# Performance work log

Measured on AMD Instinct MI355X. Metric: run time of the kernel, lower is better.

## Reference

```python
import jax, jax.numpy as jnp
import numpy as np

N, D, H, C, L, G, E = 50000, 128, 128, 40, 3, 4, 800000
GRID = jnp.linspace(-2.0, 2.0, G)          # RBF grid on [-2, 2]
DENOM = 4.0 / (G - 1)                      # (grid_max - grid_min) / (num_grids - 1)


def _layernorm(x, g, b, eps=1e-5):
    m = x.mean(-1, keepdims=True)
    v = x.var(-1, keepdims=True)
    return (x - m) * jax.lax.rsqrt(v + eps) * g + b


def _fkan(x, ln_g, ln_b, sw, bw, bb):
    # FastKANLayer: layernorm -> Gaussian RBF basis -> bias-free spline linear, + silu base update
    xn = _layernorm(x, ln_g, ln_b)
    basis = jnp.exp(-(((xn[..., None] - GRID) / DENOM) ** 2))     # [n, d, G]
    ret = basis.reshape(x.shape[0], -1) @ sw.T                    # [n, out]
    return ret + jax.nn.silu(x) @ bw.T + bb


def _gcn_prop(h, src, dst, n):
    # symmetric GCN normalization with self-loops already appended to src/dst
    deg = jax.ops.segment_sum(jnp.ones(src.shape[0], h.dtype), dst, num_segments=n)
    dis = jnp.where(deg > 0, jax.lax.rsqrt(deg), 0.0)
    norm = dis[src] * dis[dst]                                    # [e]
    return jax.ops.segment_sum(h[src] * norm[:, None], dst, num_segments=n)


def _batchnorm(x, g, b, eps=1e-5):
    m = x.mean(0)
    v = x.var(0)  # biased variance, as torch BN uses for normalization
    return (x - m) * jax.lax.rsqrt(v + eps) * g + b


def setup_inputs() -> dict:
    key = jax.random.key(0)
    ks = jax.random.split(key, 8)
    x = jax.random.normal(ks[0], (N, D), jnp.float32)
    edge_index = jax.random.randint(ks[1], (2, E), 0, N, jnp.int64)
    return {
        "x": x,
        "edge_index": edge_index,
        "ln_g": jnp.ones((L, D), jnp.float32),
        "ln_b": jnp.zeros((L, D), jnp.float32),
        "sw": jax.random.normal(ks[2], (L, H, D * G), jnp.float32) * 0.1,
        "bw": jax.random.normal(ks[3], (L, H, D), jnp.float32) * (1.0 / np.sqrt(D)),
        "bb": jnp.zeros((L, H), jnp.float32),
        "gcn_bias": jnp.zeros((L, H), jnp.float32),
        "bn_g": jnp.ones((L, H), jnp.float32),
        "bn_b": jnp.zeros((L, H), jnp.float32),
        "ln_g_out": jnp.ones((D + L * H,), jnp.float32),
        "ln_b_out": jnp.zeros((D + L * H,), jnp.float32),
        "sw_out": jax.random.normal(ks[4], (C, (D + L * H) * G), jnp.float32) * 0.1,
        "bw_out": jax.random.normal(ks[5], (C, D + L * H), jnp.float32) * (1.0 / np.sqrt(D + L * H)),
        "bb_out": jnp.zeros((C,), jnp.float32),
    }


def reference(x, edge_index, ln_g, ln_b, sw, bw, bb, gcn_bias, bn_g, bn_b,
              ln_g_out, ln_b_out, sw_out, bw_out, bb_out):
    loops = jnp.arange(N, dtype=edge_index.dtype)
    src = jnp.concatenate([edge_index[0], loops])
    dst = jnp.concatenate([edge_index[1], loops])
    feats = [x]
    h = x
    for i in range(L):  # fixed small layer count
        h = _fkan(h, ln_g[i], ln_b[i], sw[i], bw[i], bb[i])
        h = _gcn_prop(h, src, dst, N) + gcn_bias[i]
        h = _batchnorm(h, bn_g[i], bn_b[i])
        feats.append(h)
    xcat = jnp.concatenate(feats, axis=1)  # [N, D + L*H] skip-concat
    return _fkan(xcat, ln_g_out, ln_b_out, sw_out, bw_out, bb_out)
```

## Files before the change

### kernel.cpp

```cpp
#include <hip/hip_runtime.h>
#include <hip/hip_bf16.h>

#define TPB 256

typedef __attribute__((ext_vector_type(8))) short s8v;
typedef __attribute__((ext_vector_type(4))) float f32x4;
typedef unsigned short u16;

__device__ __forceinline__ u16 f2bf(float f){
  union { __hip_bfloat16 h; u16 u; } cv;
  cv.h = __float2bfloat16(f);
  return cv.u;
}

__device__ __forceinline__ unsigned pack_bf2(float lo, float hi){
  return (unsigned)f2bf(lo) | ((unsigned)f2bf(hi) << 16);
}

__device__ __forceinline__ float bflo(unsigned u){ return __uint_as_float(u << 16); }
__device__ __forceinline__ float bfhi(unsigned u){ return __uint_as_float(u & 0xffff0000u); }

__device__ __forceinline__ float wave_sum(float v){
  #pragma unroll
  for (int off=32; off>0; off>>=1) v += __shfl_xor(v, off, 64);
  return v;
}

__device__ __forceinline__ int wave_incl_scan(int v, int lane){
  #pragma unroll
  for (int off=1; off<64; off<<=1){
    int u = __shfl_up(v, off, 64);
    if (lane >= off) v += u;
  }
  return v;
}

__global__ __launch_bounds__(TPB) void count_k(const int* __restrict__ dstE, int* __restrict__ cnt, int E){
  int e = blockIdx.x*TPB + threadIdx.x;
  if (e < E) atomicAdd(&cnt[dstE[e]], 1);
}

__global__ __launch_bounds__(TPB) void dis_k(const int* __restrict__ cnt, float* __restrict__ disp, int nN){
  int n = blockIdx.x*TPB + threadIdx.x;
  if (n < nN) disp[n] = rsqrtf((float)cnt[n] + 1.0f);
}

__global__ __launch_bounds__(TPB) void scan1_k(const int* __restrict__ cnt, int* __restrict__ rowptr,
                                               int* __restrict__ bsum, int nN){
  int t = threadIdx.x;
  int i = blockIdx.x*TPB + t;
  int lane = t & 63, wid = t >> 6;
  int v = (i < nN) ? cnt[i] : 0;
  int inc = wave_incl_scan(v, lane);
  __shared__ int wsum[4];
  if (lane == 63) wsum[wid] = inc;
  __syncthreads();
  int off = 0;
  #pragma unroll
  for (int w=0; w<4; ++w) if (w < wid) off += wsum[w];
  if (i < nN) rowptr[i] = inc - v + off;
  if (t == 0) bsum[blockIdx.x] = wsum[0]+wsum[1]+wsum[2]+wsum[3];
}

__global__ __launch_bounds__(TPB) void scan2_k(int* __restrict__ bsum, int nbk){
  int t = threadIdx.x;
  int lane = t & 63, wid = t >> 6;
  int v = (t < nbk) ? bsum[t] : 0;
  int inc = wave_incl_scan(v, lane);
  __shared__ int wsum[4];
  if (lane == 63) wsum[wid] = inc;
  __syncthreads();
  int off = 0;
  #pragma unroll
  for (int w=0; w<4; ++w) if (w < wid) off += wsum[w];
  __syncthreads();
  if (t < nbk) bsum[t] = inc - v + off;
}

__global__ __launch_bounds__(TPB) void scan3_k(int* __restrict__ rowptr, const int* __restrict__ bsum, int nN, int E){
  int i = blockIdx.x*TPB + threadIdx.x;
  if (i < nN) rowptr[i] += bsum[blockIdx.x];
  if (i == 0) rowptr[nN] = E;
}

__global__ __launch_bounds__(TPB) void fill_k(const int* __restrict__ srcE, const int* __restrict__ dstE,
                                              const int* __restrict__ rowptr, int* __restrict__ cursor,
                                              int* __restrict__ csr, int E){
  int e = blockIdx.x*TPB + threadIdx.x;
  if (e >= E) return;
  int d = dstE[e];
  int pos = atomicAdd(&cursor[d], 1);
  csr[rowptr[d] + pos] = srcE[e];
}

__global__ __launch_bounds__(TPB) void ln512_k(const float* __restrict__ x, const u16* __restrict__ hl16,
                                               const float* __restrict__ scshAll,
                                               float* __restrict__ meanp, float* __restrict__ rstdp, int nN){
  int g = blockIdx.x*TPB + threadIdx.x;
  int n = g >> 6, lane = g & 63;
  if (n >= nN) return;
  float s = 0.f, sq = 0.f;
  #pragma unroll
  for (int k=0;k<8;k++){
    float v;
    if (k < 2){
      v = x[(size_t)n*128 + lane + k*64];
    } else {
      int k2 = k - 2, li = k2 >> 1, cc = lane + (k2&1)*64;
      float raw = bflo((unsigned)hl16[((size_t)li*nN + n)*128 + cc] << 0) ;
      raw = __uint_as_float(((unsigned)hl16[((size_t)li*nN + n)*128 + cc]) << 16);
      v = fmaf(raw, scshAll[li*256 + cc], scshAll[li*256 + 128 + cc]);
    }
    s += v; sq += v*v;
  }
  s = wave_sum(s); sq = wave_sum(sq);
  float m = s * (1.f/512.f);
  float var = fmaxf(sq * (1.f/512.f) - m*m, 0.f);
  if (lane == 0){ meanp[n] = m; rstdp[n] = rsqrtf(var + 1e-5f); }
}

__global__ __launch_bounds__(TPB) void prep_wpre_k(const float* __restrict__ sw, const float* __restrict__ bw,
                                                   u16* __restrict__ wpre, int IN, int KSTEPS, int NTILES, int OUTW){
  int idx = blockIdx.x*TPB + threadIdx.x;
  if (idx >= NTILES*KSTEPS*512) return;
  int b = idx & 7, lane = (idx >> 3) & 63, rest = idx >> 9;
  int kstep = rest % KSTEPS, nt = rest / KSTEPS;
  int chunk = kstep / 5, g = kstep % 5;
  int d = chunk*32 + ((lane >> 4)*8 + b);
  int n = nt*16 + (lane & 15);
  float v = 0.f;
  if (n < OUTW) v = (g < 4) ? sw[(size_t)n*IN*4 + d*4 + g] : bw[(size_t)n*IN + d];
  wpre[idx] = f2bf(v);
}

__device__ __forceinline__ void build_frags(const float* __restrict__ h8, float mean, float rstd,
                                            const float* __restrict__ lngv, const float* __restrict__ lnbv,
                                            s8v* __restrict__ a){
  float bas[5][8];
  #pragma unroll
  for (int u=0; u<8; ++u){
    float v = h8[u];
    float xn = (v - mean)*rstd*lngv[u] + lnbv[u];
    float y = 0.75f*xn;
    float z0 = y+1.5f, z1 = y+0.5f, z2 = y-0.5f, z3 = y-1.5f;
    bas[0][u] = __expf(-z0*z0);
    bas[1][u] = __expf(-z1*z1);
    bas[2][u] = __expf(-z2*z2);
    bas[3][u] = __expf(-z3*z3);
    bas[4][u] = v * __builtin_amdgcn_rcpf(1.f + __expf(-v));
  }
  #pragma unroll
  for (int g=0; g<5; ++g){
    #pragma unroll
    for (int j=0; j<4; ++j)
      ((unsigned*)&a[g])[j] = pack_bf2(bas[g][2*j], bas[g][2*j+1]);
  }
}

template<bool BF16IN>
__global__ __launch_bounds__(TPB) void fkan_layer_k(
    const float* __restrict__ in32, const u16* __restrict__ in16,
    const float* __restrict__ scsh,
    const float* __restrict__ lng, const float* __restrict__ lnb,
    const u16* __restrict__ wpre, const float* __restrict__ bias,
    const float* __restrict__ disp, u16* __restrict__ hs, int nN)
{
  const int t = threadIdx.x;
  const int wv = blockIdx.x*(TPB/64) + (t >> 6);
  const int ngrp = (nN + 15) >> 4;
  const int ng = wv >> 1, jh = wv & 1;
  if (ng >= ngrp) return;
  const int l = t & 63, clo = l & 15, kq = l >> 4;
  const int node = ng*16 + clo;
  const int nc = node < nN ? node : nN-1;

  float h[4][8];
  #pragma unroll
  for (int c=0; c<4; ++c){
    if (BF16IN){
      uint4 raw = *(const uint4*)(in16 + (size_t)nc*128 + c*32 + kq*8);
      h[c][0]=bflo(raw.x); h[c][1]=bfhi(raw.x);
      h[c][2]=bflo(raw.y); h[c][3]=bfhi(raw.y);
      h[c][4]=bflo(raw.z); h[c][5]=bfhi(raw.z);
      h[c][6]=bflo(raw.w); h[c][7]=bfhi(raw.w);
      #pragma unroll
      for (int u=0; u<8; ++u){
        int d = c*32 + kq*8 + u;
        h[c][u] = fmaf(h[c][u], scsh[d], scsh[128 + d]);
      }
    } else {
      const float* hrow = in32 + (size_t)nc*128;
      *(float4*)&h[c][0] = *(const float4*)(hrow + c*32 + kq*8);
      *(float4*)&h[c][4] = *(const float4*)(hrow + c*32 + kq*8 + 4);
    }
  }
  float s = 0.f, sq = 0.f;
  #pragma unroll
  for (int c=0; c<4; ++c)
    #pragma unroll
    for (int u=0; u<8; ++u){ float v = h[c][u]; s += v; sq += v*v; }
  s  += __shfl_xor(s, 16, 64);  s  += __shfl_xor(s, 32, 64);
  sq += __shfl_xor(sq, 16, 64); sq += __shfl_xor(sq, 32, 64);
  float mean = s * (1.f/128.f);
  float var  = fmaxf(sq * (1.f/128.f) - mean*mean, 0.f);
  float rstd = rsqrtf(var + 1e-5f);

  f32x4 acc[4];
  #pragma unroll
  for (int j=0; j<4; ++j) acc[j] = (f32x4)0.f;

  for (int c=0; c<4; ++c){
    float lngv[8], lnbv[8];
    *(float4*)&lngv[0] = *(const float4*)(lng + c*32 + kq*8);
    *(float4*)&lngv[4] = *(const float4*)(lng + c*32 + kq*8 + 4);
    *(float4*)&lnbv[0] = *(const float4*)(lnb + c*32 + kq*8);
    *(float4*)&lnbv[4] = *(const float4*)(lnb + c*32 + kq*8 + 4);
    s8v a[5];
    build_frags(h[c], mean, rstd, lngv, lnbv, a);
    #pragma unroll
    for (int ks=0; ks<5; ++ks){
      const int kglob = c*5 + ks;
      #pragma unroll
      for (int j=0; j<4; ++j){
        s8v b = *(const s8v*)(wpre + ((size_t)((jh*4 + j)*20 + kglob)*64 + l)*8);
        acc[j] = __builtin_amdgcn_mfma_f32_16x16x32_bf16(a[ks], b, acc[j], 0, 0, 0);
      }
    }
  }
  float bv[4];
  #pragma unroll
  for (int j=0; j<4; ++j) bv[j] = bias[(jh*4 + j)*16 + clo];
  #pragma unroll
  for (int rr=0; rr<4; ++rr){
    int nw = ng*16 + kq*4 + rr;
    if (nw < nN){
      float dsc = disp[nw];
      #pragma unroll
      for (int j=0; j<4; ++j)
        hs[(size_t)nw*128 + (jh*4 + j)*16 + clo] = f2bf((acc[j][rr] + bv[j]) * dsc);
    }
  }
}

__global__ __launch_bounds__(TPB) void fkan_out_k(
    const float* __restrict__ x, const u16* __restrict__ hl16,
    const float* __restrict__ scshAll,
    const float* __restrict__ meanp, const float* __restrict__ rstdp,
    const float* __restrict__ lng, const float* __restrict__ lnb,
    const u16* __restrict__ wpre, const float* __restrict__ bias,
    float* __restrict__ out, int nN)
{
  __shared__ float sred[4][24][64];
  const int t = threadIdx.x;
  const int w = t >> 6, l = t & 63, clo = l & 15, kq = l >> 4;
  const int nb0 = blockIdx.x * 32;
  int nc0 = nb0 + clo;      nc0 = nc0 < nN ? nc0 : nN-1;
  int nc1 = nb0 + 16 + clo; nc1 = nc1 < nN ? nc1 : nN-1;
  const float mean0 = meanp[nc0], rstd0 = rstdp[nc0];
  const float mean1 = meanp[nc1], rstd1 = rstdp[nc1];

  f32x4 acc[2][3];
  #pragma unroll
  for (int m=0; m<2; ++m)
    #pragma unroll
    for (int j=0; j<3; ++j) acc[m][j] = (f32x4)0.f;

  #pragma unroll
  for (int cc=0; cc<4; ++cc){
    const int c = w*4 + cc;
    const int d0 = c*32 + kq*8;
    float lngv[8], lnbv[8];
    *(float4*)&lngv[0] = *(const float4*)(lng + d0);
    *(float4*)&lngv[4] = *(const float4*)(lng + d0 + 4);
    *(float4*)&lnbv[0] = *(const float4*)(lnb + d0);
    *(float4*)&lnbv[4] = *(const float4*)(lnb + d0 + 4);
    float h0[8], h1[8];
    if (d0 < 128){
      const float* s0 = x + (size_t)nc0*128 + d0;
      const float* s1 = x + (size_t)nc1*128 + d0;
      *(float4*)&h0[0] = *(const float4*)(s0);  *(float4*)&h0[4] = *(const float4*)(s0+4);
      *(float4*)&h1[0] = *(const float4*)(s1);  *(float4*)&h1[4] = *(const float4*)(s1+4);
    } else {
      int dd = d0 - 128, li = dd >> 7, cc2 = dd & 127;
      uint4 r0 = *(const uint4*)(hl16 + ((size_t)li*nN + nc0)*128 + cc2);
      uint4 r1 = *(const uint4*)(hl16 + ((size_t)li*nN + nc1)*128 + cc2);
      h0[0]=bflo(r0.x); h0[1]=bfhi(r0.x); h0[2]=bflo(r0.y); h0[3]=bfhi(r0.y);
      h0[4]=bflo(r0.z); h0[5]=bfhi(r0.z); h0[6]=bflo(r0.w); h0[7]=bfhi(r0.w);
      h1[0]=bflo(r1.x); h1[1]=bfhi(r1.x); h1[2]=bflo(r1.y); h1[3]=bfhi(r1.y);
      h1[4]=bflo(r1.z); h1[5]=bfhi(r1.z); h1[6]=bflo(r1.w); h1[7]=bfhi(r1.w);
      #pragma unroll
      for (int u=0; u<8; ++u){
        float sc = scshAll[li*256 + cc2 + u], sh = scshAll[li*256 + 128 + cc2 + u];
        h0[u] = fmaf(h0[u], sc, sh);
        h1[u] = fmaf(h1[u], sc, sh);
      }
    }
    s8v a0[5], a1[5];
    build_frags(h0, mean0, rstd0, lngv, lnbv, a0);
    build_frags(h1, mean1, rstd1, lngv, lnbv, a1);
    #pragma unroll
    for (int ks=0; ks<5; ++ks){
      const int kglob = c*5 + ks;
      #pragma unroll
      for (int j=0; j<3; ++j){
        s8v b = *(const s8v*)(wpre + ((size_t)(j*80 + kglob)*64 + l)*8);
        acc[0][j] = __builtin_amdgcn_mfma_f32_16x16x32_bf16(a0[ks], b, acc[0][j], 0, 0, 0);
        acc[1][j] = __builtin_amdgcn_mfma_f32_16x16x32_bf16(a1[ks], b, acc[1][j], 0, 0, 0);
      }
    }
  }
  #pragma unroll
  for (int m=0; m<2; ++m)
    #pragma unroll
    for (int j=0; j<3; ++j)
      #pragma unroll
      for (int rr=0; rr<4; ++rr)
        sred[w][m*12 + j*4 + rr][l] = acc[m][j][rr];
  __syncthreads();
  #pragma unroll
  for (int k=0; k<6; ++k){
    int q = t + k*256;
    int slot = q >> 6, l2 = q & 63;
    float val = sred[0][slot][l2] + sred[1][slot][l2] + sred[2][slot][l2] + sred[3][slot][l2];
    int m = slot >= 12 ? 1 : 0;
    int jrr = slot - m*12;
    int j = jrr >> 2, rr = jrr & 3;
    int nodeq = nb0 + m*16 + (l2 >> 4)*4 + rr;
    int col = j*16 + (l2 & 15);
    if (nodeq < nN && col < 40)
      out[(size_t)nodeq*40 + col] = val + bias[col];
  }
}

__device__ __forceinline__ void acc_bf4(uint2 u, float& a0, float& a1, float& a2, float& a3){
  a0 += bflo(u.x); a1 += bfhi(u.x);
  a2 += bflo(u.y); a3 += bfhi(u.y);
}

__global__ __launch_bounds__(TPB) void gcn_k(const u16* __restrict__ hs, const int* __restrict__ rowptr,
                                             const int* __restrict__ csr, const float* __restrict__ disp,
                                             u16* __restrict__ hl, int nN){
  int g = blockIdx.x*TPB + threadIdx.x;
  int n = g >> 6, lane = g & 63;
  if (n >= nN) return;
  const uint2* H2 = (const uint2*)hs;
  const int li = lane & 31, half = lane >> 5;
  int e0 = rowptr[n], e1 = rowptr[n+1];
  float a0=0.f, a1=0.f, a2=0.f, a3=0.f;
  for (int base = e0; base < e1; base += 8){
    int r[4];
    #pragma unroll
    for (int k=0; k<4; ++k){
      int idx = base + half*4 + k;
      int idc = idx < e1 ? idx : e0;
      int rv  = csr[idc];
      r[k] = idx < e1 ? rv : nN;
    }
    #pragma unroll
    for (int k=0; k<4; ++k){
      uint2 u = H2[(size_t)r[k]*32 + li];
      acc_bf4(u, a0, a1, a2, a3);
    }
  }
  a0 += __shfl_xor(a0, 32, 64);
  a1 += __shfl_xor(a1, 32, 64);
  a2 += __shfl_xor(a2, 32, 64);
  a3 += __shfl_xor(a3, 32, 64);
  if (half == 0){
    uint2 u = H2[(size_t)n*32 + li];
    acc_bf4(u, a0, a1, a2, a3);
    float dn = disp[n];
    uint2 o;
    o.x = pack_bf2(a0*dn, a1*dn);
    o.y = pack_bf2(a2*dn, a3*dn);
    *(uint2*)(hl + (size_t)n*128 + li*4) = o;
  }
}

__global__ __launch_bounds__(TPB) void bn_stat_k(const u16* __restrict__ hl, float* __restrict__ stats, int nN){
  int cp   = threadIdx.x & 63;
  int strm = threadIdx.x >> 6;
  const unsigned* H = (const unsigned*)hl;
  float s0=0.f, s1=0.f, q0=0.f, q1=0.f;
  for (int r = blockIdx.x*4 + strm; r < nN; r += gridDim.x*4){
    unsigned u = H[(size_t)r*64 + cp];
    float lo = bflo(u), hi = bfhi(u);
    s0 += lo; q0 += lo*lo; s1 += hi; q1 += hi*hi;
  }
  __shared__ float ls[4][64][4];
  ls[strm][cp][0] = s0; ls[strm][cp][1] = q0; ls[strm][cp][2] = s1; ls[strm][cp][3] = q1;
  __syncthreads();
  if (strm == 0){
    float S0 = ls[0][cp][0]+ls[1][cp][0]+ls[2][cp][0]+ls[3][cp][0];
    float Q0 = ls[0][cp][1]+ls[1][cp][1]+ls[2][cp][1]+ls[3][cp][1];
    float S1 = ls[0][cp][2]+ls[1][cp][2]+ls[2][cp][2]+ls[3][cp][2];
    float Q1 = ls[0][cp][3]+ls[1][cp][3]+ls[2][cp][3]+ls[3][cp][3];
    atomicAdd(&stats[cp*2],       S0);
    atomicAdd(&stats[cp*2+1],     S1);
    atomicAdd(&stats[128+cp*2],   Q0);
    atomicAdd(&stats[128+cp*2+1], Q1);
  }
}

__global__ void bn_fin_k(const float* __restrict__ stats, const float* __restrict__ g, const float* __restrict__ b,
                         float* __restrict__ scsh, int nN){
  int c = threadIdx.x;
  float inv = 1.f/(float)nN;
  float m = stats[c]*inv;
  float var = fmaxf(stats[128+c]*inv - m*m, 0.f);
  float sc = g[c]*rsqrtf(var + 1e-5f);
  scsh[c] = sc;
  scsh[128+c] = b[c] - m*sc;
}

extern "C" void kernel_launch(void* const* d_in, const int* in_sizes, int n_in,
                              void* d_out, int out_size, void* d_ws, size_t ws_size,
                              hipStream_t stream)
{
  const float* x        = (const float*)d_in[0];
  const int*   ei       = (const int*)d_in[1];
  const float* ln_g     = (const float*)d_in[2];
  const float* ln_b     = (const float*)d_in[3];
  const float* sw       = (const float*)d_in[4];
  const float* bw       = (const float*)d_in[5];
  const float* bb       = (const float*)d_in[6];
  const float* bn_g     = (const float*)d_in[8];
  const float* bn_b     = (const float*)d_in[9];
  const float* ln_g_out = (const float*)d_in[10];
  const float* ln_b_out = (const float*)d_in[11];
  const float* sw_out   = (const float*)d_in[12];
  const float* bw_out   = (const float*)d_in[13];
  const float* bb_out   = (const float*)d_in[14];
  float* out = (float*)d_out;

  const int nN = in_sizes[0] / 128;
  const int E  = in_sizes[1] / 2;

  char* ws = (char*)d_ws;
  size_t off = 0;
  auto alloc = [&](size_t bytes)->char*{
    char* p = ws + off; off = (off + bytes + 255) & ~size_t(255); return p;
  };
  u16*   hl16  = (u16*)alloc((size_t)3*nN*128*2);
  u16*   hs    = (u16*)alloc((size_t)(nN+1)*128*2);
  float* meanp = (float*)alloc((size_t)nN*4);
  float* rstdp = (float*)alloc((size_t)nN*4);
  float* disp  = (float*)alloc((size_t)nN*4);
  float* stats = (float*)alloc(256*4);
  float* scshL = (float*)alloc(3*256*4);
  u16*   wpreL = (u16*)alloc((size_t)3*8*20*512*2);
  u16*   wpreO = (u16*)alloc((size_t)3*80*512*2);
  int* cnt     = (int*)alloc((size_t)nN*4);
  int* cursor  = (int*)alloc((size_t)nN*4);
  int* rowptr  = (int*)alloc((size_t)(nN+1)*4);
  int* bsum    = (int*)alloc(256*4);
  int* csr     = (int*)alloc((size_t)E*4);
  (void)ws_size; (void)n_in; (void)out_size;

  const int* srcE = ei;
  const int* dstE = ei + E;

  hipMemsetAsync(cnt, 0, (size_t)nN*4, stream);
  hipMemsetAsync(cursor, 0, (size_t)nN*4, stream);
  hipMemsetAsync(hs + (size_t)nN*128, 0, 256, stream);

  for (int i=0; i<3; ++i)
    prep_wpre_k<<<(8*20*512 + TPB-1)/TPB, TPB, 0, stream>>>(
        sw + (size_t)i*128*512, bw + (size_t)i*128*128, wpreL + (size_t)i*8*20*512, 128, 20, 8, 128);
  prep_wpre_k<<<(3*80*512 + TPB-1)/TPB, TPB, 0, stream>>>(
      sw_out, bw_out, wpreO, 512, 80, 3, 40);

  const int nbE = (E + TPB-1)/TPB;
  const int nbN = (nN + TPB-1)/TPB;
  count_k<<<nbE, TPB, 0, stream>>>(dstE, cnt, E);
  dis_k<<<nbN, TPB, 0, stream>>>(cnt, disp, nN);
  scan1_k<<<nbN, TPB, 0, stream>>>(cnt, rowptr, bsum, nN);
  scan2_k<<<1, TPB, 0, stream>>>(bsum, nbN);
  scan3_k<<<nbN, TPB, 0, stream>>>(rowptr, bsum, nN, E);
  fill_k<<<nbE, TPB, 0, stream>>>(srcE, dstE, rowptr, cursor, csr, E);

  const int nbW = (nN*64 + TPB-1)/TPB;
  const int nbL = (((nN + 15)/16)*2 + 3)/4;
  const int nbO = (nN + 31)/32;

  for (int i=0; i<3; ++i){
    if (i == 0){
      fkan_layer_k<false><<<nbL, TPB, 0, stream>>>(
          x, (const u16*)nullptr, (const float*)nullptr,
          ln_g, ln_b, wpreL, bb, disp, hs, nN);
    } else {
      fkan_layer_k<true><<<nbL, TPB, 0, stream>>>(
          (const float*)nullptr, hl16 + (size_t)(i-1)*nN*128, scshL + (size_t)(i-1)*256,
          ln_g + (size_t)i*128, ln_b + (size_t)i*128,
          wpreL + (size_t)i*8*20*512, bb + (size_t)i*128, disp, hs, nN);
    }
    gcn_k<<<nbW, TPB, 0, stream>>>(hs, rowptr, csr, disp, hl16 + (size_t)i*nN*128, nN);
    hipMemsetAsync(stats, 0, 256*4, stream);
    bn_stat_k<<<256, TPB, 0, stream>>>(hl16 + (size_t)i*nN*128, stats, nN);
    bn_fin_k<<<1, 128, 0, stream>>>(stats, bn_g + (size_t)i*128, bn_b + (size_t)i*128,
                                    scshL + (size_t)i*256, nN);
  }

  ln512_k<<<nbW, TPB, 0, stream>>>(x, hl16, scshL, meanp, rstdp, nN);
  fkan_out_k<<<nbO, TPB, 0, stream>>>(
      x, hl16, scshL, meanp, rstdp, ln_g_out, ln_b_out, wpreO, bb_out, out, nN);
}
```

Baseline: 456.1 us.

## Widen GCN gather loads, split output FKAN over 8 waves, use exp2 basis

New measurement: 438.4 us. 3.9% less time.

```diff
diff --git a/kernel.cpp b/kernel.cpp
--- a/kernel.cpp
+++ b/kernel.cpp
@@ -2,6 +2,7 @@
 #include <hip/hip_bf16.h>
 
 #define TPB 256
+#define TPBO 512
 
 typedef __attribute__((ext_vector_type(8))) short s8v;
 typedef __attribute__((ext_vector_type(4))) float f32x4;
@@ -107,8 +108,7 @@
       v = x[(size_t)n*128 + lane + k*64];
     } else {
       int k2 = k - 2, li = k2 >> 1, cc = lane + (k2&1)*64;
-      float raw = bflo((unsigned)hl16[((size_t)li*nN + n)*128 + cc] << 0) ;
-      raw = __uint_as_float(((unsigned)hl16[((size_t)li*nN + n)*128 + cc]) << 16);
+      float raw = __uint_as_float(((unsigned)hl16[((size_t)li*nN + n)*128 + cc]) << 16);
       v = fmaf(raw, scshAll[li*256 + cc], scshAll[li*256 + 128 + cc]);
     }
     s += v; sq += v*v;
@@ -141,13 +141,17 @@
   for (int u=0; u<8; ++u){
     float v = h8[u];
     float xn = (v - mean)*rstd*lngv[u] + lnbv[u];
-    float y = 0.75f*xn;
-    float z0 = y+1.5f, z1 = y+0.5f, z2 = y-0.5f, z3 = y-1.5f;
-    bas[0][u] = __expf(-z0*z0);
-    bas[1][u] = __expf(-z1*z1);
-    bas[2][u] = __expf(-z2*z2);
-    bas[3][u] = __expf(-z3*z3);
-    bas[4][u] = v * __builtin_amdgcn_rcpf(1.f + __expf(-v));
+    float y = 0.900841806f*xn;
+    float d0 = y + 1.80168361f;
+    float d1 = y + 0.600561204f;
+    float d2 = y - 0.600561204f;
+    float d3 = y - 1.80168361f;
+    bas[0][u] = __builtin_amdgcn_exp2f(-d0*d0);
+    bas[1][u] = __builtin_amdgcn_exp2f(-d1*d1);
+    bas[2][u] = __builtin_amdgcn_exp2f(-d2*d2);
+    bas[3][u] = __builtin_amdgcn_exp2f(-d3*d3);
+    float e = __builtin_amdgcn_exp2f(-1.44269504f*v);
+    bas[4][u] = v * __builtin_amdgcn_rcpf(1.f + e);
   }
   #pragma unroll
   for (int g=0; g<5; ++g){
@@ -242,7 +246,7 @@
   }
 }
 
-__global__ __launch_bounds__(TPB) void fkan_out_k(
+__global__ __launch_bounds__(TPBO) void fkan_out_k(
     const float* __restrict__ x, const u16* __restrict__ hl16,
     const float* __restrict__ scshAll,
     const float* __restrict__ meanp, const float* __restrict__ rstdp,
@@ -250,7 +254,7 @@
     const u16* __restrict__ wpre, const float* __restrict__ bias,
     float* __restrict__ out, int nN)
 {
-  __shared__ float sred[4][24][64];
+  __shared__ float sred[8][24][64];
   const int t = threadIdx.x;
   const int w = t >> 6, l = t & 63, clo = l & 15, kq = l >> 4;
   const int nb0 = blockIdx.x * 32;
@@ -266,8 +270,8 @@
     for (int j=0; j<3; ++j) acc[m][j] = (f32x4)0.f;
 
   #pragma unroll
-  for (int cc=0; cc<4; ++cc){
-    const int c = w*4 + cc;
+  for (int cc=0; cc<2; ++cc){
+    const int c = w*2 + cc;
     const int d0 = c*32 + kq*8;
     float lngv[8], lnbv[8];
     *(float4*)&lngv[0] = *(const float4*)(lng + d0);
@@ -318,10 +322,12 @@
         sred[w][m*12 + j*4 + rr][l] = acc[m][j][rr];
   __syncthreads();
   #pragma unroll
-  for (int k=0; k<6; ++k){
-    int q = t + k*256;
+  for (int k=0; k<3; ++k){
+    int q = t + k*TPBO;
     int slot = q >> 6, l2 = q & 63;
-    float val = sred[0][slot][l2] + sred[1][slot][l2] + sred[2][slot][l2] + sred[3][slot][l2];
+    float val = 0.f;
+    #pragma unroll
+    for (int ww=0; ww<8; ++ww) val += sred[ww][slot][l2];
     int m = slot >= 12 ? 1 : 0;
     int jrr = slot - m*12;
     int j = jrr >> 2, rr = jrr & 3;
@@ -332,9 +338,11 @@
   }
 }
 
-__device__ __forceinline__ void acc_bf4(uint2 u, float& a0, float& a1, float& a2, float& a3){
-  a0 += bflo(u.x); a1 += bfhi(u.x);
-  a2 += bflo(u.y); a3 += bfhi(u.y);
+__device__ __forceinline__ void acc_bf8(uint4 u, float* __restrict__ a){
+  a[0] += bflo(u.x); a[1] += bfhi(u.x);
+  a[2] += bflo(u.y); a[3] += bfhi(u.y);
+  a[4] += bflo(u.z); a[5] += bfhi(u.z);
+  a[6] += bflo(u.w); a[7] += bfhi(u.w);
 }
 
 __global__ __launch_bounds__(TPB) void gcn_k(const u16* __restrict__ hs, const int* __restrict__ rowptr,
@@ -343,37 +351,42 @@
   int g = blockIdx.x*TPB + threadIdx.x;
   int n = g >> 6, lane = g & 63;
   if (n >= nN) return;
-  const uint2* H2 = (const uint2*)hs;
-  const int li = lane & 31, half = lane >> 5;
+  const uint4* H4 = (const uint4*)hs;
+  const int li = lane & 15, qd = lane >> 4;
   int e0 = rowptr[n], e1 = rowptr[n+1];
-  float a0=0.f, a1=0.f, a2=0.f, a3=0.f;
-  for (int base = e0; base < e1; base += 8){
+  float a[8];
+  #pragma unroll
+  for (int j=0; j<8; ++j) a[j] = 0.f;
+  for (int base = e0; base < e1; base += 16){
     int r[4];
     #pragma unroll
     for (int k=0; k<4; ++k){
-      int idx = base + half*4 + k;
-      int idc = idx < e1 ? idx : e0;
+      int idx = base + qd*4 + k;
+      int idc = idx < e1 ? idx : e1-1;
       int rv  = csr[idc];
       r[k] = idx < e1 ? rv : nN;
     }
     #pragma unroll
     for (int k=0; k<4; ++k){
-      uint2 u = H2[(size_t)r[k]*32 + li];
-      acc_bf4(u, a0, a1, a2, a3);
-    }
-  }
-  a0 += __shfl_xor(a0, 32, 64);
-  a1 += __shfl_xor(a1, 32, 64);
-  a2 += __shfl_xor(a2, 32, 64);
-  a3 += __shfl_xor(a3, 32, 64);
-  if (half == 0){
-    uint2 u = H2[(size_t)n*32 + li];
-    acc_bf4(u, a0, a1, a2, a3);
+      uint4 u = H4[(size_t)r[k]*16 + li];
+      acc_bf8(u, a);
+    }
+  }
+  #pragma unroll
+  for (int j=0; j<8; ++j){
+    a[j] += __shfl_xor(a[j], 16, 64);
+    a[j] += __shfl_xor(a[j], 32, 64);
+  }
+  if (qd == 0){
+    uint4 u = H4[(size_t)n*16 + li];
+    acc_bf8(u, a);
     float dn = disp[n];
-    uint2 o;
-    o.x = pack_bf2(a0*dn, a1*dn);
-    o.y = pack_bf2(a2*dn, a3*dn);
-    *(uint2*)(hl + (size_t)n*128 + li*4) = o;
+    uint4 o;
+    o.x = pack_bf2(a[0]*dn, a[1]*dn);
+    o.y = pack_bf2(a[2]*dn, a[3]*dn);
+    o.z = pack_bf2(a[4]*dn, a[5]*dn);
+    o.w = pack_bf2(a[6]*dn, a[7]*dn);
+    *(uint4*)(hl + (size_t)n*128 + li*8) = o;
   }
 }
 
@@ -502,6 +515,6 @@
   }
 
   ln512_k<<<nbW, TPB, 0, stream>>>(x, hl16, scshL, meanp, rstdp, nN);
-  fkan_out_k<<<nbO, TPB, 0, stream>>>(
+  fkan_out_k<<<nbO, TPBO, 0, stream>>>(
       x, hl16, scshL, meanp, rstdp, ln_g_out, ln_b_out, wpreO, bb_out, out, nN);
 }
```
